# Kernel optimization log

Measured on AMD Instinct MI355X. Metric: run time of the kernel, lower is better.

Reference implementation:

```python
import jax, jax.numpy as jnp
import numpy as np

N_NODES = 100000
N_EDGES = 3200000
N_GRAPHS = 512


def setup_inputs() -> dict:
    key = jax.random.key(0)
    k1, k2, k3, k4, k5 = jax.random.split(key, 5)
    x = jax.random.normal(k1, (N_NODES, 5), dtype=jnp.float32)
    edge_index = jax.random.randint(k2, (2, N_EDGES), 0, N_NODES, dtype=jnp.int64)
    batch = jnp.sort(jax.random.randint(k3, (N_NODES,), 0, N_GRAPHS, dtype=jnp.int64))
    W1 = jax.random.normal(k4, (5, 16), dtype=jnp.float32) * (1.0 / np.sqrt(5.0))
    b1 = jnp.zeros((16,), dtype=jnp.float32)
    W2 = jax.random.normal(k5, (16, 16), dtype=jnp.float32) * 0.25
    b2 = jnp.zeros((16,), dtype=jnp.float32)
    return {"x": x, "edge_index": edge_index, "batch": batch,
            "W1": W1, "b1": b1, "W2": W2, "b2": b2}


def _gcn_conv(x, src, dst, norm, W, b, n_nodes):
    # PyG GCNConv: h = X W; out_i = sum_{j->i} norm_ij * h_j + b
    h = x @ W                                   # [N, out]
    msgs = h[src] * norm[:, None]               # gather + scale  [E_tot, out]
    out = jax.ops.segment_sum(msgs, dst, num_segments=n_nodes)
    return out + b


def reference(x, edge_index, batch, W1, b1, W2, b2):
    n = x.shape[0]
    # add self-loops (GCNConv default)
    loops = jnp.arange(n, dtype=edge_index.dtype)
    src = jnp.concatenate([edge_index[0], loops])
    dst = jnp.concatenate([edge_index[1], loops])
    # symmetric normalization: deg computed on destination nodes
    deg = jax.ops.segment_sum(jnp.ones_like(src, dtype=x.dtype), dst, num_segments=n)
    dinv = jnp.where(deg > 0, jax.lax.rsqrt(deg), 0.0)
    norm = dinv[src] * dinv[dst]                # [E_tot]

    h = jax.nn.relu(_gcn_conv(x, src, dst, norm, W1, b1, n))
    h = jax.nn.relu(_gcn_conv(h, src, dst, norm, W2, b2, n))

    # global mean pool over graphs in the batch
    sums = jax.ops.segment_sum(h, batch, num_segments=N_GRAPHS)
    cnts = jax.ops.segment_sum(jnp.ones((n,), dtype=h.dtype), batch, num_segments=N_GRAPHS)
    return sums / jnp.maximum(cnts, 1.0)[:, None]
```

## Files before the change

kernel.cpp:

```cpp
#include <hip/hip_runtime.h>

#define N_NODES  100000
#define N_EDGES  3200000
#define N_GRAPHS 512
#define F_IN     5
#define F_HID    16

#define PBLK   512
#define CHUNK  2048
#define NCHUNK ((N_EDGES + CHUNK - 1) / CHUNK)
#define BKT_NODES 256
#define NBKT ((N_NODES + BKT_NODES - 1) / BKT_NODES)
#define SHARDS 8
#define CAP_S  1280
#define CAP    (SHARDS * CAP_S)


__device__ inline unsigned short f2bf(float f) {
    unsigned u = __float_as_uint(f);
    return (unsigned short)((u + 0x7fffu + ((u >> 16) & 1u)) >> 16);
}
__device__ inline float bf2f(unsigned short h) {
    return __uint_as_float(((unsigned)h) << 16);
}
__device__ inline float4 cvt4(ushort4 u) {
    return make_float4(bf2f(u.x), bf2f(u.y), bf2f(u.z), bf2f(u.w));
}
__device__ inline float4 shfl_xor4(float4 v, int m) {
    return make_float4(__shfl_xor(v.x, m, 64), __shfl_xor(v.y, m, 64),
                       __shfl_xor(v.z, m, 64), __shfl_xor(v.w, m, 64));
}

template <int NW>
__device__ inline int block_incl_scan(int v, int t, int* wsum) {
    int lane = t & 63, wave = t >> 6;
    int x = v;
#pragma unroll
    for (int o = 1; o < 64; o <<= 1) {
        int y = __shfl_up(x, o, 64);
        if (lane >= o) x += y;
    }
    if (lane == 63) wsum[wave] = x;
    __syncthreads();
    if (t < 64) {
        int w = (t < NW) ? wsum[t] : 0;
#pragma unroll
        for (int o = 1; o < NW; o <<= 1) {
            int y = __shfl_up(w, o, 64);
            if (t >= o) w += y;
        }
        if (t < NW) wsum[t] = w;
    }
    __syncthreads();
    return x + (wave ? wsum[wave - 1] : 0);
}

__device__ inline float4 row_gather8s(const ushort4* __restrict__ pb4, int i, int j,
                                      int half, int beg, int len,
                                      const int* __restrict__ col) {
    float4 acc = half ? make_float4(0.f, 0.f, 0.f, 0.f)
                      : cvt4(pb4[i * 4 + j]);
    for (int k = half * 8; k < len; k += 16) {
        int4 c0 = *(const int4*)(col + beg + k);
        int4 c1 = *(const int4*)(col + beg + k + 4);
        ushort4 a0 = pb4[c0.x * 4 + j], a1 = pb4[c0.y * 4 + j];
        ushort4 a2 = pb4[c0.z * 4 + j], a3 = pb4[c0.w * 4 + j];
        ushort4 a4 = pb4[c1.x * 4 + j], a5 = pb4[c1.y * 4 + j];
        ushort4 a6 = pb4[c1.z * 4 + j], a7 = pb4[c1.w * 4 + j];
        float4 f0 = cvt4(a0), f1 = cvt4(a1), f2 = cvt4(a2), f3 = cvt4(a3);
        float4 f4 = cvt4(a4), f5 = cvt4(a5), f6 = cvt4(a6), f7 = cvt4(a7);
        acc.x += ((f0.x + f1.x) + (f2.x + f3.x)) + ((f4.x + f5.x) + (f6.x + f7.x));
        acc.y += ((f0.y + f1.y) + (f2.y + f3.y)) + ((f4.y + f5.y) + (f6.y + f7.y));
        acc.z += ((f0.z + f1.z) + (f2.z + f3.z)) + ((f4.z + f5.z) + (f6.z + f7.z));
        acc.w += ((f0.w + f1.w) + (f2.w + f3.w)) + ((f4.w + f5.w) + (f6.w + f7.w));
    }
    return acc;
}


__global__ void k_zero(int* __restrict__ cursor, float* __restrict__ out,
                       float* __restrict__ cnt, unsigned short* __restrict__ pb_a,
                       unsigned short* __restrict__ pb_b) {
    int i = blockIdx.x * blockDim.x + threadIdx.x;
    if (i < NBKT * SHARDS) cursor[i] = 0;
    if (i < N_GRAPHS * F_HID) out[i] = 0.0f;
    if (i < N_GRAPHS) cnt[i] = 0.0f;
    if (i < F_HID) {
        pb_a[(size_t)N_NODES * F_HID + i] = 0;
        pb_b[(size_t)N_NODES * F_HID + i] = 0;
    }
}

__global__ __launch_bounds__(PBLK) void k_part(const int* __restrict__ src,
                                               const int* __restrict__ dst,
                                               const int* __restrict__ batch,
                                               int* __restrict__ cursor,
                                               unsigned* __restrict__ packed,
                                               float* __restrict__ cnt) {
    __shared__ int hist[PBLK];
    __shared__ int scn[PBLK];
    __shared__ int rnk[PBLK];
    __shared__ int gbase[PBLK];
    __shared__ int wsum[8];
    __shared__ int bcnt[8];
    __shared__ int g0s;
    int t = threadIdx.x;
    int blk = blockIdx.x;
    int s = blk & (SHARDS - 1);
    int chunk0 = blk * CHUNK;
    int n = min(CHUNK, N_EDGES - chunk0);
    hist[t] = 0;
    if (t < 8) bcnt[t] = 0;
    if (t == 0 && blk < NBKT) {
        int nb = blk * BKT_NODES;
        g0s = batch[nb < N_NODES ? nb : N_NODES - 1];
    }
    __syncthreads();
    int ls[CHUNK / PBLK], ld[CHUNK / PBLK];
#pragma unroll
    for (int idx = 0; idx < CHUNK / PBLK; idx++) {
        int k = t + idx * PBLK;
        if (k < n) {
            ls[idx] = src[chunk0 + k];
            ld[idx] = dst[chunk0 + k];
            atomicAdd(&hist[ld[idx] >> 8], 1);
        }
    }
    if (blk < NBKT && t < BKT_NODES) {
        int i2 = blk * BKT_NODES + t;
        if (i2 < N_NODES) {
            int g = batch[i2];
            int l = g - g0s;
            if (l >= 0 && l < 8) atomicAdd(&bcnt[l], 1);
            else atomicAdd(&cnt[g], 1.0f);
        }
    }
    __syncthreads();
    int v = hist[t];
    int incl = block_incl_scan<8>(v, t, wsum);
    int excl = incl - v;
    scn[t] = excl;
    rnk[t] = excl;
    gbase[t] = (v > 0) ? atomicAdd(&cursor[t * SHARDS + s], v) : 0;
    if (blk < NBKT && t < 8 && bcnt[t] > 0) atomicAdd(&cnt[g0s + t], (float)bcnt[t]);
    __syncthreads();
#pragma unroll
    for (int idx = 0; idx < CHUNK / PBLK; idx++) {
        int k = t + idx * PBLK;
        if (k < n) {
            int d = ld[idx], sr = ls[idx];
            int b = d >> 8;
            int r = atomicAdd(&rnk[b], 1);
            int g = gbase[b] + (r - scn[b]);
            if (g < CAP_S)
                packed[(size_t)b * CAP + s * CAP_S + g] =
                    ((unsigned)sr << 8) | (unsigned)(d & 255);
        }
    }
}

__global__ __launch_bounds__(512) void k_csr(const int* __restrict__ cursor,
                                             const unsigned* __restrict__ packed,
                                             const float* __restrict__ x,
                                             const float* __restrict__ W1,
                                             int2* __restrict__ rowbc,
                                             int* __restrict__ col,
                                             float* __restrict__ dinv,
                                             unsigned short* __restrict__ pb) {
    __shared__ int hist[BKT_NODES];
    __shared__ int rnk[BKT_NODES];
    __shared__ int wsum[8];
    __shared__ int ns[SHARDS];
    __shared__ float w1[F_IN * F_HID];
    __shared__ unsigned pkd[CAP];
    int b = blockIdx.x, t = threadIdx.x;
    int base = b * CAP;
    if (t < BKT_NODES) hist[t] = 0;
    if (t < SHARDS) ns[t] = min(cursor[b * SHARDS + t], CAP_S);
    if (t >= 512 - F_IN * F_HID) w1[t - (512 - F_IN * F_HID)] = W1[t - (512 - F_IN * F_HID)];
    __syncthreads();
    int sgr[SHARDS], tot = 0;
#pragma unroll
    for (int s = 0; s < SHARDS; s++) { sgr[s] = tot; tot += ns[s]; }
    const unsigned* pk = packed + (size_t)b * CAP;
#pragma unroll
    for (int s = 0; s < SHARDS; s++) {
        int m = ns[s];
        const unsigned* pks = pk + s * CAP_S;
        int sg = sgr[s];
        for (int k = t; k < m; k += 512) {
            unsigned u = pks[k];
            pkd[sg + k] = u;
            atomicAdd(&hist[u & 255], 1);
        }
    }
    __syncthreads();
    int v = (t < BKT_NODES) ? hist[t] : 0;
    int len = (v + 7) & ~7;
    int incl = block_incl_scan<8>(len, t, wsum);
    int excl = incl - len;
    if (t < BKT_NODES) rnk[t] = excl;
    __syncthreads();
    for (int e = t; e < tot; e += 512) {
        unsigned w = pkd[e];
        int r = atomicAdd(&rnk[w & 255], 1);
        if (r < CAP) col[base + r] = (int)(w >> 8);
    }
    if (t < BKT_NODES) {
        int node = b * BKT_NODES + t;
        if (node < N_NODES) {
            int mylen = min(len, ((CAP - min(excl, CAP)) & ~7));
            for (int q = v; q < mylen; q++) {
                int r = excl + q;
                if (r < CAP) col[base + r] = N_NODES;
            }
            rowbc[node] = make_int2(base + excl, mylen);
            float di = rsqrtf((float)(1 + v));
            dinv[node] = di;
            float xi[F_IN];
#pragma unroll
            for (int k = 0; k < F_IN; k++) xi[k] = x[node * F_IN + k];
            float hv[F_HID];
#pragma unroll
            for (int c = 0; c < F_HID; c++) {
                float h = 0.0f;
#pragma unroll
                for (int k = 0; k < F_IN; k++) h += xi[k] * w1[k * F_HID + c];
                hv[c] = h * di;
            }
            unsigned pkk[8];
#pragma unroll
            for (int q = 0; q < 8; q++)
                pkk[q] = (unsigned)f2bf(hv[2 * q]) | ((unsigned)f2bf(hv[2 * q + 1]) << 16);
            uint4* d4 = (uint4*)(pb + (size_t)node * F_HID);
            d4[0] = make_uint4(pkk[0], pkk[1], pkk[2], pkk[3]);
            d4[1] = make_uint4(pkk[4], pkk[5], pkk[6], pkk[7]);
        }
    }
}

__global__ __launch_bounds__(256) void k_pull_mid(const int2* __restrict__ rowbc,
                                                  const int* __restrict__ col,
                                                  const unsigned short* __restrict__ pb,
                                                  const float* __restrict__ dinv,
                                                  const float* __restrict__ W2,
                                                  const float* __restrict__ b1,
                                                  unsigned short* __restrict__ pb2) {
    __shared__ float w[F_HID * F_HID];
    __shared__ float bb[F_HID];
    int t = threadIdx.x;
    w[t] = W2[t];
    if (t < F_HID) bb[t] = b1[t];
    __syncthreads();
    int gid = blockIdx.x * 256 + t;
    int i = gid >> 3;
    int half = (gid >> 2) & 1;
    int j = gid & 3;
    int2 rc = rowbc[i];
    float4 acc = row_gather8s((const ushort4*)pb, i, j, half, rc.x, rc.y, col);
    acc.x += __shfl_xor(acc.x, 4, 64);
    acc.y += __shfl_xor(acc.y, 4, 64);
    acc.z += __shfl_xor(acc.z, 4, 64);
    acc.w += __shfl_xor(acc.w, 4, 64);
    float di = dinv[i];
    float4 mine;
    mine.x = fmaxf(di * acc.x + bb[4 * j + 0], 0.0f);
    mine.y = fmaxf(di * acc.y + bb[4 * j + 1], 0.0f);
    mine.z = fmaxf(di * acc.z + bb[4 * j + 2], 0.0f);
    mine.w = fmaxf(di * acc.w + bb[4 * j + 3], 0.0f);
    float4 o1 = shfl_xor4(mine, 1);
    float4 o2 = shfl_xor4(mine, 2);
    float4 o3 = shfl_xor4(mine, 3);
    float4 hq0 = (j == 0) ? mine : ((j == 1) ? o1 : ((j == 2) ? o2 : o3));
    float4 hq1 = (j == 1) ? mine : ((j == 0) ? o1 : ((j == 3) ? o2 : o3));
    float4 hq2 = (j == 2) ? mine : ((j == 3) ? o1 : ((j == 0) ? o2 : o3));
    float4 hq3 = (j == 3) ? mine : ((j == 2) ? o1 : ((j == 1) ? o2 : o3));
    float hc[F_HID] = {hq0.x, hq0.y, hq0.z, hq0.w, hq1.x, hq1.y, hq1.z, hq1.w,
                       hq2.x, hq2.y, hq2.z, hq2.w, hq3.x, hq3.y, hq3.z, hq3.w};
    float m0 = 0.0f, m1 = 0.0f, m2 = 0.0f, m3 = 0.0f;
#pragma unroll
    for (int c = 0; c < F_HID; c++) {
        float4 wv = *(const float4*)&w[c * F_HID + 4 * j];
        float hv = hc[c];
        m0 += hv * wv.x; m1 += hv * wv.y; m2 += hv * wv.z; m3 += hv * wv.w;
    }
    if (half == 0) {
        unsigned p0 = (unsigned)f2bf(m0 * di) | ((unsigned)f2bf(m1 * di) << 16);
        unsigned p1 = (unsigned)f2bf(m2 * di) | ((unsigned)f2bf(m3 * di) << 16);
        *(uint2*)(pb2 + (size_t)i * F_HID + 4 * j) = make_uint2(p0, p1);
    }
}

__global__ __launch_bounds__(256) void k_pull_pool(const int2* __restrict__ rowbc,
                                                   const int* __restrict__ col,
                                                   const unsigned short* __restrict__ pb,
                                                   const float* __restrict__ dinv,
                                                   const int* __restrict__ batch,
                                                   const float* __restrict__ b2,
                                                   const float* __restrict__ cnt,
                                                   float* __restrict__ out) {
    __shared__ float bb[F_HID];
    __shared__ float acc2[8][F_HID];
    __shared__ int gcnt[8];
    __shared__ int g0s;
    int t = threadIdx.x;
    if (t < F_HID) bb[t] = b2[t];
    if (t < 8) gcnt[t] = 0;
    if (t < 8 * F_HID) ((float*)acc2)[t] = 0.0f;
    int blk0node = blockIdx.x * 32;
    if (t == 0) g0s = batch[blk0node < N_NODES ? blk0node : N_NODES - 1];
    __syncthreads();
    int g0 = g0s;
    int gid = blockIdx.x * 256 + t;
    int i = gid >> 3;
    int half = (gid >> 2) & 1;
    int j = gid & 3;
    int2 rc = rowbc[i];
    float4 acc = row_gather8s((const ushort4*)pb, i, j, half, rc.x, rc.y, col);
    acc.x += __shfl_xor(acc.x, 4, 64);
    acc.y += __shfl_xor(acc.y, 4, 64);
    acc.z += __shfl_xor(acc.z, 4, 64);
    acc.w += __shfl_xor(acc.w, 4, 64);
    if (half == 0) {
        float di = dinv[i];
        float h0 = fmaxf(di * acc.x + bb[4 * j + 0], 0.0f);
        float h1 = fmaxf(di * acc.y + bb[4 * j + 1], 0.0f);
        float h2 = fmaxf(di * acc.z + bb[4 * j + 2], 0.0f);
        float h3 = fmaxf(di * acc.w + bb[4 * j + 3], 0.0f);
        int g = batch[i];
        int l = g - g0;
        if (l >= 0 && l < 8) {
            atomicAdd(&acc2[l][4 * j + 0], h0);
            atomicAdd(&acc2[l][4 * j + 1], h1);
            atomicAdd(&acc2[l][4 * j + 2], h2);
            atomicAdd(&acc2[l][4 * j + 3], h3);
            if (j == 0) atomicAdd(&gcnt[l], 1);
        } else {
            float inv = 1.0f / cnt[g];
            atomicAdd(&out[g * F_HID + 4 * j + 0], h0 * inv);
            atomicAdd(&out[g * F_HID + 4 * j + 1], h1 * inv);
            atomicAdd(&out[g * F_HID + 4 * j + 2], h2 * inv);
            atomicAdd(&out[g * F_HID + 4 * j + 3], h3 * inv);
        }
    }
    __syncthreads();
    if (t < 8 * F_HID) {
        int l = t >> 4, c = t & 15;
        if (gcnt[l] > 0) {
            float inv = 1.0f / cnt[g0 + l];
            atomicAdd(&out[(g0 + l) * F_HID + c], acc2[l][c] * inv);
        }
    }
}


extern "C" void kernel_launch(void* const* d_in, const int* in_sizes, int n_in,
                              void* d_out, int out_size, void* d_ws, size_t ws_size,
                              hipStream_t stream) {
    const float* x     = (const float*)d_in[0];
    const int*   ei    = (const int*)d_in[1];
    const int*   batch = (const int*)d_in[2];
    const float* W1    = (const float*)d_in[3];
    const float* b1    = (const float*)d_in[4];
    const float* W2    = (const float*)d_in[5];
    const float* b2    = (const float*)d_in[6];
    float* out = (float*)d_out;

    int*            cursor = (int*)d_ws;
    unsigned*       packed = (unsigned*)(cursor + 3200);
    int2*           rowbc  = (int2*)(packed + (size_t)NBKT * CAP);
    int*            col    = (int*)(rowbc + N_NODES);
    float*          dinv   = (float*)(col + (size_t)NBKT * CAP);
    unsigned short* pb_a   = (unsigned short*)(dinv + N_NODES);
    unsigned short* pb_b   = pb_a + (size_t)(N_NODES + 1) * F_HID;
    float*          cnt    = (float*)(pb_b + (size_t)(N_NODES + 1) * F_HID);

    const int* src = ei;
    const int* dst = ei + N_EDGES;

    const int nb_pull = (N_NODES * 8) / 256;

    k_zero<<<(N_GRAPHS * F_HID + 255) / 256, 256, 0, stream>>>(cursor, out, cnt,
                                                               pb_a, pb_b);
    k_part<<<NCHUNK, PBLK, 0, stream>>>(src, dst, batch, cursor, packed, cnt);
    k_csr<<<NBKT, 512, 0, stream>>>(cursor, packed, x, W1, rowbc, col, dinv, pb_a);
    k_pull_mid<<<nb_pull, 256, 0, stream>>>(rowbc, col, pb_a, dinv, W2, b1, pb_b);
    k_pull_pool<<<nb_pull, 256, 0, stream>>>(rowbc, col, pb_b, dinv, batch, b2,
                                             cnt, out);
}
```

Baseline: 200.5 us.

## Replace atomic-cursor sharded partition with count/scan/scatter radix pass

Splits the edge partition into three kernels. A histogram pass counts edges per bucket for each 4096-edge chunk, a scan pass computes per-chunk exclusive offsets for every bucket, and a scatter pass locally sorts each chunk in shared memory before writing contiguous runs to the packed buffer. This removes the global atomic cursors and the 8-way shard layout, so k_csr reads one contiguous segment per bucket and global writes coalesce better. The cost is reading dst twice, two extra launches and a strided column scan over the H matrix. Edges still drop silently past CAP, now per bucket rather than per shard.

```diff
diff --git a/kernel.cpp b/kernel.cpp
--- a/kernel.cpp
+++ b/kernel.cpp
@@ -7,13 +7,12 @@
 #define F_HID    16
 
 #define PBLK   512
-#define CHUNK  2048
-#define NCHUNK ((N_EDGES + CHUNK - 1) / CHUNK)
+#define CHUNK  4096
+#define NBLK   ((N_EDGES + CHUNK - 1) / CHUNK)
 #define BKT_NODES 256
 #define NBKT ((N_NODES + BKT_NODES - 1) / BKT_NODES)
-#define SHARDS 8
-#define CAP_S  1280
-#define CAP    (SHARDS * CAP_S)
+#define HPAD   512
+#define CAP    10240
 
 
 __device__ inline unsigned short f2bf(float f) {
@@ -78,11 +77,10 @@
 }
 
 
-__global__ void k_zero(int* __restrict__ cursor, float* __restrict__ out,
-                       float* __restrict__ cnt, unsigned short* __restrict__ pb_a,
+__global__ void k_zero(float* __restrict__ out, float* __restrict__ cnt,
+                       unsigned short* __restrict__ pb_a,
                        unsigned short* __restrict__ pb_b) {
     int i = blockIdx.x * blockDim.x + threadIdx.x;
-    if (i < NBKT * SHARDS) cursor[i] = 0;
     if (i < N_GRAPHS * F_HID) out[i] = 0.0f;
     if (i < N_GRAPHS) cnt[i] = 0.0f;
     if (i < F_HID) {
@@ -91,24 +89,16 @@
     }
 }
 
-__global__ __launch_bounds__(PBLK) void k_part(const int* __restrict__ src,
-                                               const int* __restrict__ dst,
-                                               const int* __restrict__ batch,
-                                               int* __restrict__ cursor,
-                                               unsigned* __restrict__ packed,
-                                               float* __restrict__ cnt) {
-    __shared__ int hist[PBLK];
-    __shared__ int scn[PBLK];
-    __shared__ int rnk[PBLK];
-    __shared__ int gbase[PBLK];
-    __shared__ int wsum[8];
+__global__ __launch_bounds__(PBLK) void k_count(const int* __restrict__ dst,
+                                                const int* __restrict__ batch,
+                                                int* __restrict__ H,
+                                                float* __restrict__ cnt) {
+    __shared__ int hist[HPAD];
     __shared__ int bcnt[8];
     __shared__ int g0s;
-    int t = threadIdx.x;
-    int blk = blockIdx.x;
-    int s = blk & (SHARDS - 1);
+    int t = threadIdx.x, blk = blockIdx.x;
     int chunk0 = blk * CHUNK;
-    int n = min(CHUNK, N_EDGES - chunk0);
+    int n4 = min(CHUNK, N_EDGES - chunk0) >> 2;
     hist[t] = 0;
     if (t < 8) bcnt[t] = 0;
     if (t == 0 && blk < NBKT) {
@@ -116,14 +106,16 @@
         g0s = batch[nb < N_NODES ? nb : N_NODES - 1];
     }
     __syncthreads();
-    int ls[CHUNK / PBLK], ld[CHUNK / PBLK];
-#pragma unroll
-    for (int idx = 0; idx < CHUNK / PBLK; idx++) {
-        int k = t + idx * PBLK;
-        if (k < n) {
-            ls[idx] = src[chunk0 + k];
-            ld[idx] = dst[chunk0 + k];
-            atomicAdd(&hist[ld[idx] >> 8], 1);
+    const int4* d4 = (const int4*)(dst + chunk0);
+#pragma unroll
+    for (int i = 0; i < CHUNK / 4 / PBLK; i++) {
+        int k = t + i * PBLK;
+        if (k < n4) {
+            int4 d = d4[k];
+            atomicAdd(&hist[d.x >> 8], 1);
+            atomicAdd(&hist[d.y >> 8], 1);
+            atomicAdd(&hist[d.z >> 8], 1);
+            atomicAdd(&hist[d.w >> 8], 1);
         }
     }
     if (blk < NBKT && t < BKT_NODES) {
@@ -136,30 +128,102 @@
         }
     }
     __syncthreads();
+    H[blk * HPAD + t] = hist[t];
+    if (blk < NBKT && t < 8 && bcnt[t] > 0) atomicAdd(&cnt[g0s + t], (float)bcnt[t]);
+}
+
+__global__ __launch_bounds__(256) void k_scan(int* __restrict__ H,
+                                              int* __restrict__ cnt_b) {
+    __shared__ int wsum[8];
+    int b = blockIdx.x, t = threadIdx.x;
+    int v[4];
+    int s = 0;
+#pragma unroll
+    for (int i = 0; i < 4; i++) {
+        int pos = t * 4 + i;
+        v[i] = (pos < NBLK) ? H[pos * HPAD + b] : 0;
+        s += v[i];
+    }
+    int incl = block_incl_scan<4>(s, t, wsum);
+    int run = incl - s;
+#pragma unroll
+    for (int i = 0; i < 4; i++) {
+        int pos = t * 4 + i;
+        if (pos < NBLK) H[pos * HPAD + b] = run;
+        run += v[i];
+    }
+    if (t == 255) cnt_b[b] = incl;
+}
+
+__global__ __launch_bounds__(PBLK) void k_scatter(const int* __restrict__ src,
+                                                  const int* __restrict__ dst,
+                                                  const int* __restrict__ H,
+                                                  unsigned* __restrict__ packed) {
+    __shared__ int hist[HPAD];
+    __shared__ int scn[HPAD];
+    __shared__ int rnk[HPAD];
+    __shared__ int base[HPAD];
+    __shared__ int wsum[8];
+    __shared__ unsigned pkd[CHUNK];
+    __shared__ unsigned short bkt[CHUNK];
+    int t = threadIdx.x, blk = blockIdx.x;
+    int chunk0 = blk * CHUNK;
+    int n = min(CHUNK, N_EDGES - chunk0);
+    int n4 = n >> 2;
+    hist[t] = 0;
+    base[t] = H[blk * HPAD + t];
+    __syncthreads();
+    const int4* s4 = (const int4*)(src + chunk0);
+    const int4* d4 = (const int4*)(dst + chunk0);
+    int4 lsv[CHUNK / 4 / PBLK], ldv[CHUNK / 4 / PBLK];
+#pragma unroll
+    for (int i = 0; i < CHUNK / 4 / PBLK; i++) {
+        int k = t + i * PBLK;
+        if (k < n4) {
+            lsv[i] = s4[k];
+            ldv[i] = d4[k];
+            atomicAdd(&hist[ldv[i].x >> 8], 1);
+            atomicAdd(&hist[ldv[i].y >> 8], 1);
+            atomicAdd(&hist[ldv[i].z >> 8], 1);
+            atomicAdd(&hist[ldv[i].w >> 8], 1);
+        }
+    }
+    __syncthreads();
     int v = hist[t];
     int incl = block_incl_scan<8>(v, t, wsum);
     int excl = incl - v;
     scn[t] = excl;
     rnk[t] = excl;
-    gbase[t] = (v > 0) ? atomicAdd(&cursor[t * SHARDS + s], v) : 0;
-    if (blk < NBKT && t < 8 && bcnt[t] > 0) atomicAdd(&cnt[g0s + t], (float)bcnt[t]);
-    __syncthreads();
-#pragma unroll
-    for (int idx = 0; idx < CHUNK / PBLK; idx++) {
-        int k = t + idx * PBLK;
-        if (k < n) {
-            int d = ld[idx], sr = ls[idx];
-            int b = d >> 8;
-            int r = atomicAdd(&rnk[b], 1);
-            int g = gbase[b] + (r - scn[b]);
-            if (g < CAP_S)
-                packed[(size_t)b * CAP + s * CAP_S + g] =
-                    ((unsigned)sr << 8) | (unsigned)(d & 255);
-        }
-    }
-}
-
-__global__ __launch_bounds__(512) void k_csr(const int* __restrict__ cursor,
+    __syncthreads();
+#pragma unroll
+    for (int i = 0; i < CHUNK / 4 / PBLK; i++) {
+        int k = t + i * PBLK;
+        if (k < n4) {
+            int ds0 = ldv[i].x, ds1 = ldv[i].y, ds2 = ldv[i].z, ds3 = ldv[i].w;
+            int ss0 = lsv[i].x, ss1 = lsv[i].y, ss2 = lsv[i].z, ss3 = lsv[i].w;
+            int b0 = ds0 >> 8, b1 = ds1 >> 8, b2 = ds2 >> 8, b3 = ds3 >> 8;
+            int r0 = atomicAdd(&rnk[b0], 1);
+            pkd[r0] = ((unsigned)ss0 << 8) | (unsigned)(ds0 & 255);
+            bkt[r0] = (unsigned short)b0;
+            int r1 = atomicAdd(&rnk[b1], 1);
+            pkd[r1] = ((unsigned)ss1 << 8) | (unsigned)(ds1 & 255);
+            bkt[r1] = (unsigned short)b1;
+            int r2 = atomicAdd(&rnk[b2], 1);
+            pkd[r2] = ((unsigned)ss2 << 8) | (unsigned)(ds2 & 255);
+            bkt[r2] = (unsigned short)b2;
+            int r3 = atomicAdd(&rnk[b3], 1);
+            pkd[r3] = ((unsigned)ss3 << 8) | (unsigned)(ds3 & 255);
+            bkt[r3] = (unsigned short)b3;
+        }
+    }
+    __syncthreads();
+    for (int p = t; p < n; p += PBLK) {
+        int b = bkt[p];
+        packed[(size_t)b * CAP + base[b] + (p - scn[b])] = pkd[p];
+    }
+}
+
+__global__ __launch_bounds__(512) void k_csr(const int* __restrict__ cnt_b,
                                              const unsigned* __restrict__ packed,
                                              const float* __restrict__ x,
                                              const float* __restrict__ W1,
@@ -170,29 +234,21 @@
     __shared__ int hist[BKT_NODES];
     __shared__ int rnk[BKT_NODES];
     __shared__ int wsum[8];
-    __shared__ int ns[SHARDS];
+    __shared__ int tots;
     __shared__ float w1[F_IN * F_HID];
     __shared__ unsigned pkd[CAP];
     int b = blockIdx.x, t = threadIdx.x;
     int base = b * CAP;
     if (t < BKT_NODES) hist[t] = 0;
-    if (t < SHARDS) ns[t] = min(cursor[b * SHARDS + t], CAP_S);
+    if (t == 0) tots = min(cnt_b[b], CAP);
     if (t >= 512 - F_IN * F_HID) w1[t - (512 - F_IN * F_HID)] = W1[t - (512 - F_IN * F_HID)];
     __syncthreads();
-    int sgr[SHARDS], tot = 0;
-#pragma unroll
-    for (int s = 0; s < SHARDS; s++) { sgr[s] = tot; tot += ns[s]; }
+    int tot = tots;
     const unsigned* pk = packed + (size_t)b * CAP;
-#pragma unroll
-    for (int s = 0; s < SHARDS; s++) {
-        int m = ns[s];
-        const unsigned* pks = pk + s * CAP_S;
-        int sg = sgr[s];
-        for (int k = t; k < m; k += 512) {
-            unsigned u = pks[k];
-            pkd[sg + k] = u;
-            atomicAdd(&hist[u & 255], 1);
-        }
+    for (int k = t; k < tot; k += 512) {
+        unsigned u = pk[k];
+        pkd[k] = u;
+        atomicAdd(&hist[u & 255], 1);
     }
     __syncthreads();
     int v = (t < BKT_NODES) ? hist[t] : 0;
@@ -366,8 +422,9 @@
     const float* b2    = (const float*)d_in[6];
     float* out = (float*)d_out;
 
-    int*            cursor = (int*)d_ws;
-    unsigned*       packed = (unsigned*)(cursor + 3200);
+    int*            H      = (int*)d_ws;
+    int*            cnt_b  = H + (size_t)NBLK * HPAD;
+    unsigned*       packed = (unsigned*)(cnt_b + 512);
     int2*           rowbc  = (int2*)(packed + (size_t)NBKT * CAP);
     int*            col    = (int*)(rowbc + N_NODES);
     float*          dinv   = (float*)(col + (size_t)NBKT * CAP);
@@ -380,10 +437,11 @@
 
     const int nb_pull = (N_NODES * 8) / 256;
 
-    k_zero<<<(N_GRAPHS * F_HID + 255) / 256, 256, 0, stream>>>(cursor, out, cnt,
-                                                               pb_a, pb_b);
-    k_part<<<NCHUNK, PBLK, 0, stream>>>(src, dst, batch, cursor, packed, cnt);
-    k_csr<<<NBKT, 512, 0, stream>>>(cursor, packed, x, W1, rowbc, col, dinv, pb_a);
+    k_zero<<<(N_GRAPHS * F_HID + 255) / 256, 256, 0, stream>>>(out, cnt, pb_a, pb_b);
+    k_count<<<NBLK, PBLK, 0, stream>>>(dst, batch, H, cnt);
+    k_scan<<<NBKT, 256, 0, stream>>>(H, cnt_b);
+    k_scatter<<<NBLK, PBLK, 0, stream>>>(src, dst, H, packed);
+    k_csr<<<NBKT, 512, 0, stream>>>(cnt_b, packed, x, W1, rowbc, col, dinv, pb_a);
     k_pull_mid<<<nb_pull, 256, 0, stream>>>(rowbc, col, pb_a, dinv, W2, b1, pb_b);
     k_pull_pool<<<nb_pull, 256, 0, stream>>>(rowbc, col, pb_b, dinv, batch, b2,
                                              cnt, out);
```

New measurement: 175.4 us. 1.14x faster.
